# Performance work log

Hardware: AMD Instinct MI355X
Metric: run time of the kernel (lower is better)

## Reference

```python
import math
import jax, jax.numpy as jnp
import numpy as np

B, L, D, H = 4, 2048, 512, 8
DK = D // H  # d_keys = d_values = 64
KFAC = 3


def setup_inputs() -> dict:
    key = jax.random.key(0)
    ks = jax.random.split(key, 10)
    u_part = min(KFAC * int(math.ceil(math.log(L))), L)  # 24
    scale = 1.0 / math.sqrt(D)
    return {
        "queries": jax.random.normal(ks[0], (B, L, D), jnp.float32),
        "keys": jax.random.normal(ks[1], (B, L, D), jnp.float32),
        "values": jax.random.normal(ks[2], (B, L, D), jnp.float32),
        "index_sample": jax.random.randint(ks[3], (L, u_part), 0, L, jnp.int32),
        "Wq": jax.random.normal(ks[4], (D, D), jnp.float32) * scale,
        "bq": jnp.zeros((D,), jnp.float32),
        "Wk": jax.random.normal(ks[5], (D, D), jnp.float32) * scale,
        "bk": jnp.zeros((D,), jnp.float32),
        "Wv": jax.random.normal(ks[6], (D, D), jnp.float32) * scale,
        "bv": jnp.zeros((D,), jnp.float32),
        "Wo": jax.random.normal(ks[7], (D, D), jnp.float32) * scale,
        "bo": jnp.zeros((D,), jnp.float32),
    }


def reference(queries, keys, values, index_sample, Wq, bq, Wk, bk, Wv, bv, Wo, bo):
    b, q_len, d_out = queries.shape
    k_len = keys.shape[1]
    # projections -> [B, H, L, DK]
    q = (queries @ Wq + bq).reshape(b, q_len, H, DK).transpose(0, 2, 1, 3)
    k = (keys @ Wk + bk).reshape(b, k_len, H, DK).transpose(0, 2, 1, 3)
    v = (values @ Wv + bv).reshape(b, k_len, H, DK).transpose(0, 2, 1, 3)

    n_top = min(KFAC * int(math.ceil(math.log(q_len))), q_len)  # u

    # --- _prob_qk: sampled QK scores to pick sparse queries ---
    # k_sample: [B, H, q_len, sample_k, DK]
    k_sample = k[:, :, index_sample, :]
    q_k_sample = jnp.einsum("bhld,bhlsd->bhls", q, k_sample)
    m = jnp.max(q_k_sample, axis=-1) - jnp.sum(q_k_sample, axis=-1) / k_len
    _, m_top = jax.lax.top_k(m, n_top)  # [B, H, u]

    q_reduce = jnp.take_along_axis(q, m_top[..., None], axis=2)  # [B, H, u, DK]
    scores_top = jnp.einsum("bhud,bhkd->bhuk", q_reduce, k) / math.sqrt(d_out)

    # --- masked (causal) branch: mask_flag=True ---
    causal = jnp.triu(jnp.ones((q_len, k_len), bool), 1)
    indicator = causal[m_top]  # [B, H, u, k_len]
    scores_top = jnp.where(indicator, -jnp.inf, scores_top)

    attn = jax.nn.softmax(scores_top, axis=-1)  # [B, H, u, k_len]
    context = jnp.cumsum(v, axis=2)  # default context for non-selected queries
    attn_values = jnp.einsum("bhuk,bhkd->bhud", attn, v)

    bidx = jnp.arange(b)[:, None, None]
    hidx = jnp.arange(H)[None, :, None]
    context = context.at[bidx, hidx, m_top].set(attn_values)

    # mix=False: transpose back to [B, L, H, DV] then merge heads
    context = context.transpose(0, 2, 1, 3).reshape(b, q_len, H * DK)
    out = context @ Wo + bo  # dropout_rate=0 / inference: identity
    return out
```

## Files before the change

### kernel.cpp

```cpp
#include <hip/hip_runtime.h>
#include <hip/hip_bf16.h>
#include <math.h>

#define Bq 4
#define Lq 2048
#define Dq 512
#define Hq 8
#define DKq 64
#define Uq 24
#define TSCAN 16
#define NTILE (Lq / TSCAN)
#define NSUP 16
#define JCH 256
#define NCH (Lq / JCH)
#define TKCH 8

typedef unsigned short ushort_t;
typedef unsigned long long u64;
typedef __attribute__((ext_vector_type(8))) short bfrag8;
typedef __attribute__((ext_vector_type(4))) float facc4;

__device__ inline ushort_t bf16_rne(float f) {
  unsigned u = __float_as_uint(f);
  u += 0x7FFF + ((u >> 16) & 1);
  return (ushort_t)(u >> 16);
}
__device__ inline float bf16f(ushort_t h) {
  return __uint_as_float(((unsigned)h) << 16);
}
__device__ inline unsigned fkey(float f) {
  unsigned u = __float_as_uint(f);
  return (u & 0x80000000u) ? ~u : (u | 0x80000000u);
}
__device__ __forceinline__ void gl2lds16(const void* g, void* l) {
  __builtin_amdgcn_global_load_lds(
      (const __attribute__((address_space(1))) unsigned*)g,
      (__attribute__((address_space(3))) unsigned*)l, 16, 0, 0);
}

__global__ __launch_bounds__(256) void cast_all(
    const float* __restrict__ xq, const float* __restrict__ xk,
    const float* __restrict__ xv, ushort_t* __restrict__ qh,
    ushort_t* __restrict__ ql, ushort_t* __restrict__ kh,
    ushort_t* __restrict__ kl, ushort_t* __restrict__ vh) {
  int z = blockIdx.y;
  const float* x = z == 0 ? xq : (z == 1 ? xk : xv);
  ushort_t* hi = z == 0 ? qh : (z == 1 ? kh : vh);
  ushort_t* lo = z == 0 ? ql : kl;
  int t = blockIdx.x * 256 + threadIdx.x;
  float4 v = *(const float4*)&x[(size_t)t * 4];
  ushort_t h0 = bf16_rne(v.x), h1 = bf16_rne(v.y), h2 = bf16_rne(v.z),
           h3 = bf16_rne(v.w);
  ushort4 hh = {h0, h1, h2, h3};
  *(ushort4*)&hi[(size_t)t * 4] = hh;
  if (z < 2) {
    ushort4 ll = {bf16_rne(v.x - bf16f(h0)), bf16_rne(v.y - bf16f(h1)),
                  bf16_rne(v.z - bf16f(h2)), bf16_rne(v.w - bf16f(h3))};
    *(ushort4*)&lo[(size_t)t * 4] = ll;
  }
}

__global__ __launch_bounds__(256) void transpose_cast4(
    const float* __restrict__ W0, const float* __restrict__ W1,
    const float* __restrict__ W2, const float* __restrict__ W3,
    ushort_t* __restrict__ T0h, ushort_t* __restrict__ T0l,
    ushort_t* __restrict__ T1h, ushort_t* __restrict__ T1l,
    ushort_t* __restrict__ T2h, ushort_t* __restrict__ T3h) {
  __shared__ float tile[32][33];
  int z = blockIdx.z;
  const float* W = z == 0 ? W0 : (z == 1 ? W1 : (z == 2 ? W2 : W3));
  ushort_t* Th = z == 0 ? T0h : (z == 1 ? T1h : (z == 2 ? T2h : T3h));
  ushort_t* Tl = z == 0 ? T0l : (z == 1 ? T1l : nullptr);
  int k0 = blockIdx.x * 32, n0 = blockIdx.y * 32;
  int tx = threadIdx.x & 31, ty = threadIdx.x >> 5;
  for (int r = ty; r < 32; r += 8)
    tile[tx][r] = W[(size_t)(k0 + r) * 512 + n0 + tx];
  __syncthreads();
  for (int r = ty; r < 32; r += 8) {
    float v = tile[r][tx];
    ushort_t h = bf16_rne(v);
    Th[(size_t)(n0 + r) * 512 + k0 + tx] = h;
    if (Tl) Tl[(size_t)(n0 + r) * 512 + k0 + tx] = bf16_rne(v - bf16f(h));
  }
}

__global__ __launch_bounds__(256) void gemm_qkv(
    const ushort_t* __restrict__ Aqh, const ushort_t* __restrict__ Aql,
    const ushort_t* __restrict__ Akh, const ushort_t* __restrict__ Akl,
    const ushort_t* __restrict__ Avh,
    const ushort_t* __restrict__ Wqh, const ushort_t* __restrict__ Wql,
    const ushort_t* __restrict__ Wkh, const ushort_t* __restrict__ Wkl,
    const ushort_t* __restrict__ Wvh,
    const float* __restrict__ bq, const float* __restrict__ bk,
    const float* __restrict__ bv,
    float* __restrict__ qo, float* __restrict__ ko, float* __restrict__ vo) {
  __shared__ ushort_t Ash[128][32], Asl[128][32];
  __shared__ ushort_t Bsh[128][32], Bsl[128][32];
  int which = blockIdx.z;
  const ushort_t* Ah = which == 0 ? Aqh : (which == 1 ? Akh : Avh);
  const ushort_t* Al = which == 0 ? Aql : Akl;
  const ushort_t* Bh = which == 0 ? Wqh : (which == 1 ? Wkh : Wvh);
  const ushort_t* Bl = which == 0 ? Wql : Wkl;
  const float* bias = which == 0 ? bq : (which == 1 ? bk : bv);
  float* C = which == 0 ? qo : (which == 1 ? ko : vo);
  const bool split = which < 2;

  int bm = blockIdx.x, bn = blockIdx.y;
  int tid = threadIdx.x;
  int wave = tid >> 6, lane = tid & 63;
  int wm = (wave & 1) * 64, wn = (wave >> 1) * 64;
  int quad = lane >> 4, lm = lane & 15;
  int srow = tid >> 2;
  int slc = (((tid & 3) ^ ((tid >> 3) & 3))) * 8;
  int sphys = (tid & 3) * 8;
  int rsw = (quad ^ ((lm >> 1) & 3)) * 8;
  facc4 acc[4][4] = {};

  for (int k0 = 0; k0 < 512; k0 += 32) {
#pragma unroll
    for (int p = 0; p < 2; ++p) {
      int row = srow + p * 64;
      size_t ga = (size_t)(bm * 128 + row) * 512 + k0 + slc;
      size_t gb = (size_t)(bn * 128 + row) * 512 + k0 + slc;
      gl2lds16(&Ah[ga], &Ash[row][sphys]);
      gl2lds16(&Bh[gb], &Bsh[row][sphys]);
      if (split) {
        gl2lds16(&Al[ga], &Asl[row][sphys]);
        gl2lds16(&Bl[gb], &Bsl[row][sphys]);
      }
    }
    __syncthreads();
    bfrag8 afh[4], afl[4], bfh[4], bfl[4];
#pragma unroll
    for (int mt = 0; mt < 4; ++mt) {
      afh[mt] = *(bfrag8*)&Ash[wm + mt * 16 + lm][rsw];
      if (split) afl[mt] = *(bfrag8*)&Asl[wm + mt * 16 + lm][rsw];
    }
#pragma unroll
    for (int nt = 0; nt < 4; ++nt) {
      bfh[nt] = *(bfrag8*)&Bsh[wn + nt * 16 + lm][rsw];
      if (split) bfl[nt] = *(bfrag8*)&Bsl[wn + nt * 16 + lm][rsw];
    }
#pragma unroll
    for (int mt = 0; mt < 4; ++mt)
#pragma unroll
      for (int nt = 0; nt < 4; ++nt) {
        facc4 a = acc[mt][nt];
        a = __builtin_amdgcn_mfma_f32_16x16x32_bf16(afh[mt], bfh[nt], a, 0, 0, 0);
        if (split) {
          a = __builtin_amdgcn_mfma_f32_16x16x32_bf16(afl[mt], bfh[nt], a, 0, 0, 0);
          a = __builtin_amdgcn_mfma_f32_16x16x32_bf16(afh[mt], bfl[nt], a, 0, 0, 0);
        }
        acc[mt][nt] = a;
      }
    __syncthreads();
  }
#pragma unroll
  for (int mt = 0; mt < 4; ++mt)
#pragma unroll
    for (int nt = 0; nt < 4; ++nt) {
      int col = bn * 128 + wn + nt * 16 + lm;
      float bv2 = bias[col];
#pragma unroll
      for (int r = 0; r < 4; ++r) {
        int row = bm * 128 + wm + mt * 16 + quad * 4 + r;
        C[(size_t)row * 512 + col] = acc[mt][nt][r] + bv2;
      }
    }
}

__global__ __launch_bounds__(256) void gemm_bf16(
    const ushort_t* __restrict__ A, const ushort_t* __restrict__ Bt,
    const float* __restrict__ bias, float* __restrict__ C) {
  __shared__ ushort_t As[128][32];
  __shared__ ushort_t Bs[128][32];
  int bm = blockIdx.x, bn = blockIdx.y;
  int tid = threadIdx.x;
  int wave = tid >> 6, lane = tid & 63;
  int wm = (wave & 1) * 64, wn = (wave >> 1) * 64;
  int quad = lane >> 4, lm = lane & 15;
  int srow = tid >> 2;
  int slc = (((tid & 3) ^ ((tid >> 3) & 3))) * 8;
  int sphys = (tid & 3) * 8;
  int rsw = (quad ^ ((lm >> 1) & 3)) * 8;
  facc4 acc[4][4] = {};

  for (int k0 = 0; k0 < 512; k0 += 32) {
#pragma unroll
    for (int p = 0; p < 2; ++p) {
      int row = srow + p * 64;
      gl2lds16(&A[(size_t)(bm * 128 + row) * 512 + k0 + slc], &As[row][sphys]);
      gl2lds16(&Bt[(size_t)(bn * 128 + row) * 512 + k0 + slc], &Bs[row][sphys]);
    }
    __syncthreads();
    bfrag8 af[4], bf[4];
#pragma unroll
    for (int mt = 0; mt < 4; ++mt)
      af[mt] = *(bfrag8*)&As[wm + mt * 16 + lm][rsw];
#pragma unroll
    for (int nt = 0; nt < 4; ++nt)
      bf[nt] = *(bfrag8*)&Bs[wn + nt * 16 + lm][rsw];
#pragma unroll
    for (int mt = 0; mt < 4; ++mt)
#pragma unroll
      for (int nt = 0; nt < 4; ++nt)
        acc[mt][nt] = __builtin_amdgcn_mfma_f32_16x16x32_bf16(
            af[mt], bf[nt], acc[mt][nt], 0, 0, 0);
    __syncthreads();
  }
#pragma unroll
  for (int mt = 0; mt < 4; ++mt)
#pragma unroll
    for (int nt = 0; nt < 4; ++nt) {
      int col = bn * 128 + wn + nt * 16 + lm;
      float bv = bias[col];
#pragma unroll
      for (int r = 0; r < 4; ++r) {
        int row = bm * 128 + wm + mt * 16 + quad * 4 + r;
        C[(size_t)row * 512 + col] = acc[mt][nt][r] + bv;
      }
    }
}

__global__ __launch_bounds__(256) void compute_m(
    const float* __restrict__ q, const float* __restrict__ k,
    const int* __restrict__ idxs, float* __restrict__ m) {
  int wave = threadIdx.x >> 6, lane = threadIdx.x & 63;
  int lq = lane >> 4, dq = lane & 15;
  int slot = (blockIdx.x * 4 + wave) * 4 + lq;
  int l = slot & (Lq - 1);
  int bh = slot >> 11;
  int h = bh & (Hq - 1), b = bh >> 3;
  float4 qv = *(const float4*)&q[((size_t)b * Lq + l) * Dq + h * DKq + dq * 4];
  const float* kb = &k[(size_t)b * Lq * Dq + h * DKq + dq * 4];
  const int* ib = &idxs[l * Uq];
  float mx = -INFINITY, sm = 0.f;
#pragma unroll
  for (int s = 0; s < Uq; ++s) {
    int j = ib[s];
    float4 kv = *(const float4*)&kb[(size_t)j * Dq];
    float p = qv.x * kv.x + qv.y * kv.y + qv.z * kv.z + qv.w * kv.w;
    p += __shfl_xor(p, 1, 64);
    p += __shfl_xor(p, 2, 64);
    p += __shfl_xor(p, 4, 64);
    p += __shfl_xor(p, 8, 64);
    mx = fmaxf(mx, p);
    sm += p;
  }
  if (dq == 0) m[slot] = mx - sm * (1.0f / Lq);
}

__device__ inline void bitonic256_desc(u64* s, int tid) {
  for (int k = 2; k <= 256; k <<= 1) {
    for (int j = k >> 1; j > 0; j >>= 1) {
      int p = tid ^ j;
      u64 mine = s[tid], other = s[p];
      u64 mx = mine > other ? mine : other;
      u64 mn = mine > other ? other : mine;
      bool dir = (tid & k) == 0;
      bool lower = tid < p;
      u64 res = dir ? (lower ? mx : mn) : (lower ? mn : mx);
      __syncthreads();
      s[tid] = res;
      __syncthreads();
    }
  }
}

__global__ __launch_bounds__(256) void topk_stage1(
    const float* __restrict__ m, u64* __restrict__ cand) {
  __shared__ u64 s[256];
  int bh = blockIdx.x >> 3;
  int ch = blockIdx.x & 7;
  int tid = threadIdx.x;
  int gidx = ch * 256 + tid;
  float v = m[(size_t)bh * Lq + gidx];
  s[tid] = ((u64)fkey(v) << 32) | (u64)(Lq - 1 - gidx);
  __syncthreads();
  bitonic256_desc(s, tid);
  if (tid < Uq) cand[((size_t)bh * TKCH + ch) * Uq + tid] = s[tid];
}

__global__ __launch_bounds__(256) void topk_stage2(
    const u64* __restrict__ cand, int* __restrict__ mtop,
    int* __restrict__ repl) {
  __shared__ u64 s[256];
  __shared__ int mt[Uq];
  int bh = blockIdx.x;
  int tid = threadIdx.x;
  s[tid] = (tid < TKCH * Uq) ? cand[(size_t)bh * TKCH * Uq + tid] : 0ull;
  __syncthreads();
  bitonic256_desc(s, tid);
  if (tid < Uq) {
    int idx = Lq - 1 - (int)(s[tid] & 0xFFFFFFFFull);
    mtop[bh * Uq + tid] = idx;
    mt[tid] = idx;
  }
  __syncthreads();
  for (int l = tid; l < Lq; l += 256) {
    int u = -1;
#pragma unroll
    for (int t = 0; t < Uq; ++t)
      if (mt[t] == l) u = t;
    repl[(size_t)bh * Lq + l] = u;
  }
}

#define JT 256
#define JS 64

__global__ __launch_bounds__(256) void scores_kernel(
    const float* __restrict__ q, const float* __restrict__ k,
    const int* __restrict__ mtop, float* __restrict__ scg) {
  __shared__ float qs[Uq][DKq + 1];
  __shared__ float ks[JS][DKq + 1];
  __shared__ int i0s[Uq];
  int bh = blockIdx.y;
  int jt = blockIdx.x;
  int h = bh & (Hq - 1);
  int b = bh >> 3;
  int tid = threadIdx.x;
  if (tid < Uq) i0s[tid] = mtop[bh * Uq + tid];
  __syncthreads();
  for (int s = tid; s < Uq * 16; s += 256) {
    int u = s >> 4, qd = (s & 15) * 4;
    float4 t = *(const float4*)&q[((size_t)b * Lq + i0s[u]) * Dq + h * DKq + qd];
    qs[u][qd] = t.x; qs[u][qd + 1] = t.y; qs[u][qd + 2] = t.z; qs[u][qd + 3] = t.w;
  }
  int jp = tid & 31;
  int ug = tid >> 5;
  const float scale = 0.044194173824159216f;
  for (int sub = 0; sub < JT / JS; ++sub) {
    int jbase = jt * JT + sub * JS;
    __syncthreads();
    for (int s = tid; s < JS * 16; s += 256) {
      int j = s >> 4, qd = (s & 15) * 4;
      float4 t = *(const float4*)&k[((size_t)b * Lq + jbase + j) * Dq + h * DKq + qd];
      ks[j][qd] = t.x; ks[j][qd + 1] = t.y; ks[j][qd + 2] = t.z; ks[j][qd + 3] = t.w;
    }
    __syncthreads();
    float acc[3][2] = {};
    int j0 = jp * 2, j1 = j0 + 1;
#pragma unroll 8
    for (int d = 0; d < DKq; ++d) {
      float k0 = ks[j0][d], k1 = ks[j1][d];
#pragma unroll
      for (int uu = 0; uu < 3; ++uu) {
        float qv = qs[ug * 3 + uu][d];
        acc[uu][0] += qv * k0;
        acc[uu][1] += qv * k1;
      }
    }
#pragma unroll
    for (int uu = 0; uu < 3; ++uu) {
      int u = ug * 3 + uu;
      scg[((size_t)(bh * Uq + u)) * Lq + jbase + j0] = acc[uu][0] * scale;
      scg[((size_t)(bh * Uq + u)) * Lq + jbase + j1] = acc[uu][1] * scale;
    }
  }
}

__global__ __launch_bounds__(256) void softmax_pv_partial(
    const float* __restrict__ scg, const float* __restrict__ v,
    const int* __restrict__ mtop, float* __restrict__ pmax,
    float* __restrict__ psum, float* __restrict__ pvp) {
  int blk = blockIdx.y;
  int jc = blockIdx.x;
  int bh = blk / Uq;
  int h = bh & (Hq - 1);
  int b = bh >> 3;
  int n = mtop[blk] + 1;
  int j0 = jc * JCH;
  if (j0 >= n) return;
  int cnt = min(JCH, n - j0);
  int tid = threadIdx.x, wave = tid >> 6, lane = tid & 63;
  __shared__ float es[JCH];
  __shared__ float red[4][DKq];
  __shared__ float rr[4];

  const float* row = &scg[(size_t)blk * Lq + j0];
  float mx = (tid < cnt) ? row[tid] : -INFINITY;
#pragma unroll
  for (int off = 32; off; off >>= 1) mx = fmaxf(mx, __shfl_xor(mx, off, 64));
  if (lane == 0) rr[wave] = mx;
  __syncthreads();
  mx = fmaxf(fmaxf(rr[0], rr[1]), fmaxf(rr[2], rr[3]));
  __syncthreads();

  float e = (tid < cnt) ? __expf(row[tid] - mx) : 0.f;
  es[tid] = e;
  float sm = e;
#pragma unroll
  for (int off = 32; off; off >>= 1) sm += __shfl_xor(sm, off, 64);
  if (lane == 0) rr[wave] = sm;
  __syncthreads();

  float acc = 0.f;
  const float* vb = &v[((size_t)b * Lq + j0) * Dq + h * DKq + lane];
  int jlo = wave * 64;
  int jhi = min(jlo + 64, cnt);
#pragma unroll 4
  for (int j = jlo; j < jhi; ++j) acc += es[j] * vb[(size_t)j * Dq];
  red[wave][lane] = acc;
  __syncthreads();
  if (wave == 0) {
    if (lane == 0) {
      pmax[blk * NCH + jc] = mx;
      psum[blk * NCH + jc] = rr[0] + rr[1] + rr[2] + rr[3];
    }
    pvp[((size_t)blk * NCH + jc) * DKq + lane] =
        red[0][lane] + red[1][lane] + red[2][lane] + red[3][lane];
  }
}

__global__ __launch_bounds__(128) void tile_sum(const float* __restrict__ v,
                                                float* __restrict__ tsum) {
  int blk = blockIdx.x;
  int tile = blk & (NTILE - 1);
  int b = blk >> 7;
  int d4 = threadIdx.x;
  float4 s = {0.f, 0.f, 0.f, 0.f};
  const float* base = &v[((size_t)b * Lq + tile * TSCAN) * Dq + d4 * 4];
#pragma unroll
  for (int r = 0; r < TSCAN; ++r) {
    float4 x = *(const float4*)&base[(size_t)r * Dq];
    s.x += x.x; s.y += x.y; s.z += x.z; s.w += x.w;
  }
  *(float4*)&tsum[((size_t)b * NTILE + tile) * Dq + d4 * 4] = s;
}

__global__ __launch_bounds__(128) void stile_sum(
    const float* __restrict__ tsum, float* __restrict__ stsum) {
  int blk = blockIdx.x;
  int s = blk & (NSUP - 1);
  int b = blk >> 4;
  int d4 = threadIdx.x;
  float4 acc = {0.f, 0.f, 0.f, 0.f};
  const float* tb = &tsum[((size_t)b * NTILE + s * 8) * Dq + d4 * 4];
#pragma unroll
  for (int i = 0; i < 8; ++i) {
    float4 t = *(const float4*)&tb[(size_t)i * Dq];
    acc.x += t.x; acc.y += t.y; acc.z += t.z; acc.w += t.w;
  }
  *(float4*)&stsum[((size_t)b * NSUP + s) * Dq + d4 * 4] = acc;
}

__global__ __launch_bounds__(128) void build_context(
    const float* __restrict__ v, const float* __restrict__ tsum,
    const float* __restrict__ stsum, const int* __restrict__ repl,
    const float* __restrict__ pmax, const float* __restrict__ psum,
    const float* __restrict__ pvp, ushort_t* __restrict__ ctxh) {
  int blk = blockIdx.x;
  int tile = blk & (NTILE - 1);
  int b = blk >> 7;
  int d4 = threadIdx.x;
  int h = d4 >> 4;
  int sup = tile >> 3;
  float4 run = {0.f, 0.f, 0.f, 0.f};
  const float* sb = &stsum[(size_t)b * NSUP * Dq + d4 * 4];
  for (int s = 0; s < sup; ++s) {
    float4 t = *(const float4*)&sb[(size_t)s * Dq];
    run.x += t.x; run.y += t.y; run.z += t.z; run.w += t.w;
  }
  const float* tb = &tsum[((size_t)b * NTILE + sup * 8) * Dq + d4 * 4];
  int rem = tile & 7;
  for (int i = 0; i < rem; ++i) {
    float4 t = *(const float4*)&tb[(size_t)i * Dq];
    run.x += t.x; run.y += t.y; run.z += t.z; run.w += t.w;
  }
  const int* replb = &repl[(size_t)(b * Hq + h) * Lq + tile * TSCAN];
  const float* vb = &v[((size_t)b * Lq + tile * TSCAN) * Dq + d4 * 4];
  ushort_t* cb = &ctxh[((size_t)b * Lq + tile * TSCAN) * Dq + d4 * 4];
#pragma unroll
  for (int r = 0; r < TSCAN; ++r) {
    float4 x = *(const float4*)&vb[(size_t)r * Dq];
    run.x += x.x; run.y += x.y; run.z += x.z; run.w += x.w;
    int u = replb[r];
    float4 val = run;
    if (u >= 0) {
      int l = tile * TSCAN + r;
      int blku = (b * Hq + h) * Uq + u;
      int nc = (l + JCH) / JCH;
      float gmax = -INFINITY;
      for (int c = 0; c < nc; ++c) gmax = fmaxf(gmax, pmax[blku * NCH + c]);
      float tot = 0.f;
      float4 acc = {0.f, 0.f, 0.f, 0.f};
      for (int c = 0; c < nc; ++c) {
        float wgt = __expf(pmax[blku * NCH + c] - gmax);
        tot += psum[blku * NCH + c] * wgt;
        float4 pv = *(const float4*)&pvp[((size_t)blku * NCH + c) * DKq +
                                         (d4 & 15) * 4];
        acc.x += pv.x * wgt; acc.y += pv.y * wgt;
        acc.z += pv.z * wgt; acc.w += pv.w * wgt;
      }
      float inv = 1.0f / tot;
      val.x = acc.x * inv; val.y = acc.y * inv;
      val.z = acc.z * inv; val.w = acc.w * inv;
    }
    ushort4 o = {bf16_rne(val.x), bf16_rne(val.y), bf16_rne(val.z),
                 bf16_rne(val.w)};
    *(ushort4*)&cb[(size_t)r * Dq] = o;
  }
}

extern "C" void kernel_launch(void* const* d_in, const int* in_sizes, int n_in,
                              void* d_out, int out_size, void* d_ws,
                              size_t ws_size, hipStream_t stream) {
  const float* queries = (const float*)d_in[0];
  const float* keys    = (const float*)d_in[1];
  const float* values  = (const float*)d_in[2];
  const int*   idxs    = (const int*)d_in[3];
  const float* Wq = (const float*)d_in[4];
  const float* bq = (const float*)d_in[5];
  const float* Wk = (const float*)d_in[6];
  const float* bk = (const float*)d_in[7];
  const float* Wv = (const float*)d_in[8];
  const float* bv = (const float*)d_in[9];
  const float* Wo = (const float*)d_in[10];
  const float* bo = (const float*)d_in[11];
  float* out = (float*)d_out;

  const size_t BLD = (size_t)Bq * Lq * Dq;
  char* w = (char*)d_ws;
  float* q    = (float*)w; w += BLD * 4;
  float* k    = (float*)w; w += BLD * 4;
  float* v    = (float*)w; w += BLD * 4;
  float* scg  = (float*)w; w += (size_t)Bq * Hq * Uq * Lq * 4;
  float* m    = (float*)w; w += (size_t)Bq * Hq * Lq * 4;
  float* tsum = (float*)w; w += (size_t)Bq * NTILE * Dq * 4;
  float* stsum= (float*)w; w += (size_t)Bq * NSUP * Dq * 4;
  int* mtop   = (int*)w;   w += Bq * Hq * Uq * 4;
  int* repl   = (int*)w;   w += (size_t)Bq * Hq * Lq * 4;
  float* pmax = (float*)w; w += (size_t)Bq * Hq * Uq * NCH * 4;
  float* psum = (float*)w; w += (size_t)Bq * Hq * Uq * NCH * 4;
  float* pvp  = (float*)w; w += (size_t)Bq * Hq * Uq * NCH * DKq * 4;
  u64* cand   = (u64*)w;   w += (size_t)Bq * Hq * TKCH * Uq * 8;
  ushort_t* ctxh = (ushort_t*)w; w += BLD * 2;
  ushort_t* Aqh = (ushort_t*)w; w += BLD * 2;
  ushort_t* Aql = (ushort_t*)w; w += BLD * 2;
  ushort_t* Akh = (ushort_t*)w; w += BLD * 2;
  ushort_t* Akl = (ushort_t*)w; w += BLD * 2;
  ushort_t* Avh = (ushort_t*)w; w += BLD * 2;
  const size_t WSZ = 512 * 512;
  ushort_t* Wqh = (ushort_t*)w; w += WSZ * 2;
  ushort_t* Wql = (ushort_t*)w; w += WSZ * 2;
  ushort_t* Wkh = (ushort_t*)w; w += WSZ * 2;
  ushort_t* Wkl = (ushort_t*)w; w += WSZ * 2;
  ushort_t* Wvh = (ushort_t*)w; w += WSZ * 2;
  ushort_t* Woh = (ushort_t*)w; w += WSZ * 2;

  {
    dim3 tgrid(16, 16, 4);
    transpose_cast4<<<tgrid, 256, 0, stream>>>(Wq, Wk, Wv, Wo, Wqh, Wql, Wkh,
                                               Wkl, Wvh, Woh);
  }

  {
    dim3 cgrid(BLD / 4 / 256, 3);
    cast_all<<<cgrid, 256, 0, stream>>>(queries, keys, values, Aqh, Aql, Akh,
                                        Akl, Avh);
  }

  {
    dim3 ggrid(64, 4, 3);
    gemm_qkv<<<ggrid, 256, 0, stream>>>(Aqh, Aql, Akh, Akl, Avh, Wqh, Wql,
                                        Wkh, Wkl, Wvh, bq, bk, bv, q, k, v);
  }

  compute_m<<<(Bq * Hq * Lq) / 16, 256, 0, stream>>>(q, k, idxs, m);
  topk_stage1<<<Bq * Hq * TKCH, 256, 0, stream>>>(m, cand);
  topk_stage2<<<Bq * Hq, 256, 0, stream>>>(cand, mtop, repl);

  {
    dim3 sgrid(Lq / JT, Bq * Hq);
    scores_kernel<<<sgrid, 256, 0, stream>>>(q, k, mtop, scg);
  }
  {
    dim3 pgrid(NCH, Bq * Hq * Uq);
    softmax_pv_partial<<<pgrid, 256, 0, stream>>>(scg, v, mtop, pmax, psum, pvp);
  }

  tile_sum<<<Bq * NTILE, 128, 0, stream>>>(v, tsum);
  stile_sum<<<Bq * NSUP, 128, 0, stream>>>(tsum, stsum);
  build_context<<<Bq * NTILE, 128, 0, stream>>>(v, tsum, stsum, repl, pmax,
                                                psum, pvp, ctxh);

  {
    dim3 ggrid(64, 4);
    gemm_bf16<<<ggrid, 256, 0, stream>>>(ctxh, Woh, bo, out);
  }
}
```

Baseline: 276.4 us.

## Fuse sparse-query scores, chunk softmax and PV into one attention kernel

After: 278.5 us. No clear change (+0.7%).

```diff
diff --git a/kernel.cpp b/kernel.cpp
--- a/kernel.cpp
+++ b/kernel.cpp
@@ -13,6 +13,7 @@
 #define NSUP 16
 #define JCH 256
 #define NCH (Lq / JCH)
+#define JS 64
 #define TKCH 8
 
 typedef unsigned short ushort_t;
@@ -306,33 +307,45 @@
   }
 }
 
-#define JT 256
-#define JS 64
-
-__global__ __launch_bounds__(256) void scores_kernel(
+__global__ __launch_bounds__(256) void attn_fused(
     const float* __restrict__ q, const float* __restrict__ k,
-    const int* __restrict__ mtop, float* __restrict__ scg) {
+    const float* __restrict__ v, const int* __restrict__ mtop,
+    float* __restrict__ pmax, float* __restrict__ psum,
+    float* __restrict__ pvp) {
   __shared__ float qs[Uq][DKq + 1];
   __shared__ float ks[JS][DKq + 1];
+  __shared__ float es[Uq][JCH];
   __shared__ int i0s[Uq];
+  __shared__ int nsub_s;
   int bh = blockIdx.y;
   int jt = blockIdx.x;
-  int h = bh & (Hq - 1);
-  int b = bh >> 3;
+  int h = bh & (Hq - 1), b = bh >> 3;
   int tid = threadIdx.x;
+  int wave = tid >> 6, lane = tid & 63;
+  int j0 = jt * JCH;
+
   if (tid < Uq) i0s[tid] = mtop[bh * Uq + tid];
   __syncthreads();
+  if (tid == 0) {
+    int mx = 0;
+    for (int t = 0; t < Uq; ++t) mx = max(mx, i0s[t]);
+    int nmax = mx + 1 - j0;
+    nsub_s = nmax <= 0 ? 0 : min((nmax + JS - 1) / JS, JCH / JS);
+  }
   for (int s = tid; s < Uq * 16; s += 256) {
     int u = s >> 4, qd = (s & 15) * 4;
     float4 t = *(const float4*)&q[((size_t)b * Lq + i0s[u]) * Dq + h * DKq + qd];
     qs[u][qd] = t.x; qs[u][qd + 1] = t.y; qs[u][qd + 2] = t.z; qs[u][qd + 3] = t.w;
   }
-  int jp = tid & 31;
-  int ug = tid >> 5;
+  __syncthreads();
+  int nsub = nsub_s;
+  if (nsub == 0) return;
+
   const float scale = 0.044194173824159216f;
-  for (int sub = 0; sub < JT / JS; ++sub) {
-    int jbase = jt * JT + sub * JS;
-    __syncthreads();
+  int jp = tid & 31, ug = tid >> 5;
+  for (int sub = 0; sub < nsub; ++sub) {
+    int jbase = j0 + sub * JS;
+    if (sub) __syncthreads();
     for (int s = tid; s < JS * 16; s += 256) {
       int j = s >> 4, qd = (s & 15) * 4;
       float4 t = *(const float4*)&k[((size_t)b * Lq + jbase + j) * Dq + h * DKq + qd];
@@ -340,10 +353,10 @@
     }
     __syncthreads();
     float acc[3][2] = {};
-    int j0 = jp * 2, j1 = j0 + 1;
+    int jj0 = jp * 2, jj1 = jj0 + 1;
 #pragma unroll 8
     for (int d = 0; d < DKq; ++d) {
-      float k0 = ks[j0][d], k1 = ks[j1][d];
+      float k0 = ks[jj0][d], k1 = ks[jj1][d];
 #pragma unroll
       for (int uu = 0; uu < 3; ++uu) {
         float qv = qs[ug * 3 + uu][d];
@@ -354,62 +367,79 @@
 #pragma unroll
     for (int uu = 0; uu < 3; ++uu) {
       int u = ug * 3 + uu;
-      scg[((size_t)(bh * Uq + u)) * Lq + jbase + j0] = acc[uu][0] * scale;
-      scg[((size_t)(bh * Uq + u)) * Lq + jbase + j1] = acc[uu][1] * scale;
-    }
-  }
-}
-
-__global__ __launch_bounds__(256) void softmax_pv_partial(
-    const float* __restrict__ scg, const float* __restrict__ v,
-    const int* __restrict__ mtop, float* __restrict__ pmax,
-    float* __restrict__ psum, float* __restrict__ pvp) {
-  int blk = blockIdx.y;
-  int jc = blockIdx.x;
-  int bh = blk / Uq;
-  int h = bh & (Hq - 1);
-  int b = bh >> 3;
-  int n = mtop[blk] + 1;
-  int j0 = jc * JCH;
-  if (j0 >= n) return;
-  int cnt = min(JCH, n - j0);
-  int tid = threadIdx.x, wave = tid >> 6, lane = tid & 63;
-  __shared__ float es[JCH];
-  __shared__ float red[4][DKq];
-  __shared__ float rr[4];
-
-  const float* row = &scg[(size_t)blk * Lq + j0];
-  float mx = (tid < cnt) ? row[tid] : -INFINITY;
-#pragma unroll
-  for (int off = 32; off; off >>= 1) mx = fmaxf(mx, __shfl_xor(mx, off, 64));
-  if (lane == 0) rr[wave] = mx;
+      es[u][sub * JS + jj0] = acc[uu][0] * scale;
+      es[u][sub * JS + jj1] = acc[uu][1] * scale;
+    }
+  }
   __syncthreads();
-  mx = fmaxf(fmaxf(rr[0], rr[1]), fmaxf(rr[2], rr[3]));
-  __syncthreads();
-
-  float e = (tid < cnt) ? __expf(row[tid] - mx) : 0.f;
-  es[tid] = e;
-  float sm = e;
-#pragma unroll
-  for (int off = 32; off; off >>= 1) sm += __shfl_xor(sm, off, 64);
-  if (lane == 0) rr[wave] = sm;
-  __syncthreads();
-
-  float acc = 0.f;
-  const float* vb = &v[((size_t)b * Lq + j0) * Dq + h * DKq + lane];
-  int jlo = wave * 64;
-  int jhi = min(jlo + 64, cnt);
+
+  bool act[6];
+#pragma unroll
+  for (int t = 0; t < 6; ++t) {
+    int u = t * 4 + wave;
+    int cnt = i0s[u] + 1 - j0;
+    act[t] = cnt > 0;
+    if (!act[t]) continue;
+    if (cnt > JCH) cnt = JCH;
+    float x[4];
+    float mx = -INFINITY;
+#pragma unroll
+    for (int p = 0; p < 4; ++p) {
+      int j = p * 64 + lane;
+      float val = (j < cnt) ? es[u][j] : -INFINITY;
+      x[p] = val;
+      mx = fmaxf(mx, val);
+    }
+#pragma unroll
+    for (int off = 32; off; off >>= 1) mx = fmaxf(mx, __shfl_xor(mx, off, 64));
+    float sm = 0.f;
+#pragma unroll
+    for (int p = 0; p < 4; ++p) {
+      int j = p * 64 + lane;
+      float e = (j < cnt) ? __expf(x[p] - mx) : 0.f;
+      es[u][j] = e;
+      sm += e;
+    }
+#pragma unroll
+    for (int off = 32; off; off >>= 1) sm += __shfl_xor(sm, off, 64);
+    if (lane == 0) {
+      pmax[(bh * Uq + u) * NCH + jt] = mx;
+      psum[(bh * Uq + u) * NCH + jt] = sm;
+    }
+  }
+
+  float pacc[6] = {};
+  for (int sub = 0; sub < nsub; ++sub) {
+    int jbase = j0 + sub * JS;
+    __syncthreads();
+    for (int s = tid; s < JS * 16; s += 256) {
+      int j = s >> 4, qd = (s & 15) * 4;
+      float4 t = *(const float4*)&v[((size_t)b * Lq + jbase + j) * Dq + h * DKq + qd];
+      ks[j][qd] = t.x; ks[j][qd + 1] = t.y; ks[j][qd + 2] = t.z; ks[j][qd + 3] = t.w;
+    }
+    __syncthreads();
+#pragma unroll
+    for (int t = 0; t < 6; ++t) {
+      if (!act[t]) continue;
+      int u = t * 4 + wave;
+      float a = pacc[t];
+      const float* er = &es[u][sub * JS];
 #pragma unroll 4
-  for (int j = jlo; j < jhi; ++j) acc += es[j] * vb[(size_t)j * Dq];
-  red[wave][lane] = acc;
-  __syncthreads();
-  if (wave == 0) {
-    if (lane == 0) {
-      pmax[blk * NCH + jc] = mx;
-      psum[blk * NCH + jc] = rr[0] + rr[1] + rr[2] + rr[3];
-    }
-    pvp[((size_t)blk * NCH + jc) * DKq + lane] =
-        red[0][lane] + red[1][lane] + red[2][lane] + red[3][lane];
+      for (int j = 0; j < JS; j += 4) {
+        float4 ev = *(const float4*)&er[j];
+        a += ev.x * ks[j + 0][lane];
+        a += ev.y * ks[j + 1][lane];
+        a += ev.z * ks[j + 2][lane];
+        a += ev.w * ks[j + 3][lane];
+      }
+      pacc[t] = a;
+    }
+  }
+#pragma unroll
+  for (int t = 0; t < 6; ++t) {
+    if (!act[t]) continue;
+    int u = t * 4 + wave;
+    pvp[((size_t)(bh * Uq + u) * NCH + jt) * DKq + lane] = pacc[t];
   }
 }
 
@@ -525,7 +555,6 @@
   float* q    = (float*)w; w += BLD * 4;
   float* k    = (float*)w; w += BLD * 4;
   float* v    = (float*)w; w += BLD * 4;
-  float* scg  = (float*)w; w += (size_t)Bq * Hq * Uq * Lq * 4;
   float* m    = (float*)w; w += (size_t)Bq * Hq * Lq * 4;
   float* tsum = (float*)w; w += (size_t)Bq * NTILE * Dq * 4;
   float* stsum= (float*)w; w += (size_t)Bq * NSUP * Dq * 4;
@@ -572,12 +601,8 @@
   topk_stage2<<<Bq * Hq, 256, 0, stream>>>(cand, mtop, repl);
 
   {
-    dim3 sgrid(Lq / JT, Bq * Hq);
-    scores_kernel<<<sgrid, 256, 0, stream>>>(q, k, mtop, scg);
-  }
-  {
-    dim3 pgrid(NCH, Bq * Hq * Uq);
-    softmax_pv_partial<<<pgrid, 256, 0, stream>>>(scg, v, mtop, pmax, psum, pvp);
+    dim3 agrid(NCH, Bq * Hq);
+    attn_fused<<<agrid, 256, 0, stream>>>(q, k, v, mtop, pmax, psum, pvp);
   }
 
   tile_sum<<<Bq * NTILE, 128, 0, stream>>>(v, tsum);
```
